# Kernel tuning notes

Measured on AMD Instinct MI355X. Metric: run time of the kernel, lower is better.

The kernel has to match this reference:

```python
import jax, jax.numpy as jnp
import numpy as np


def _conv(x, w, b, stride, pad):
    # x: [N,C,H,W], w: [O,I,kh,kw]
    y = jax.lax.conv_general_dilated(
        x, w, (stride, stride), [(pad, pad), (pad, pad)],
        dimension_numbers=('NCHW', 'OIHW', 'NCHW'))
    return y + b[None, :, None, None]


def _block(x, w1, b1, w2, b2, stride):
    # BasicBlock with BN folded: conv3x3 -> relu -> conv3x3
    h = jax.nn.relu(_conv(x, w1, b1, stride, 1))
    return _conv(h, w2, b2, 1, 1)


def setup_inputs() -> dict:
    key = jax.random.key(0)
    keys = iter(jax.random.split(key, 64))

    def rn(shape):
        fan_in = int(np.prod(shape[1:])) if len(shape) > 1 else shape[0]
        return jax.random.normal(next(keys), shape, jnp.float32) * (1.0 / np.sqrt(fan_in))

    d = {}
    d['inputs'] = jax.random.normal(next(keys), (128, 3, 64, 64), jnp.float32)
    d['probs'] = jax.random.uniform(next(keys), (128, 15), jnp.float32)
    d['seed_w'] = rn((64, 3, 3, 3))
    d['seed_b'] = jnp.zeros((64,), jnp.float32)
    specs = [(64, 64), (64, 128), (128, 256)]  # (cin, cout) per group
    for g, (ci, co) in enumerate(specs):
        d[f'g{g}_ds_w'] = rn((co, ci, 1, 1))
        d[f'g{g}_ds_b'] = jnp.zeros((co,), jnp.float32)
        d[f'g{g}_b0_w1'] = rn((co, ci, 3, 3))
        d[f'g{g}_b0_b1'] = jnp.zeros((co,), jnp.float32)
        d[f'g{g}_b0_w2'] = rn((co, co, 3, 3))
        d[f'g{g}_b0_b2'] = jnp.zeros((co,), jnp.float32)
        d[f'g{g}_r_w1'] = rn((4, co, co, 3, 3))
        d[f'g{g}_r_b1'] = jnp.zeros((4, co), jnp.float32)
        d[f'g{g}_r_w2'] = rn((4, co, co, 3, 3))
        d[f'g{g}_r_b2'] = jnp.zeros((4, co), jnp.float32)
    d['fc_w'] = rn((1000, 256))
    d['fc_b'] = jnp.zeros((1000,), jnp.float32)
    return d


def reference(inputs, probs, seed_w, seed_b,
              g0_ds_w, g0_ds_b, g0_b0_w1, g0_b0_b1, g0_b0_w2, g0_b0_b2,
              g0_r_w1, g0_r_b1, g0_r_w2, g0_r_b2,
              g1_ds_w, g1_ds_b, g1_b0_w1, g1_b0_b1, g1_b0_w2, g1_b0_b2,
              g1_r_w1, g1_r_b1, g1_r_w2, g1_r_b2,
              g2_ds_w, g2_ds_b, g2_b0_w1, g2_b0_b1, g2_b0_w2, g2_b0_b2,
              g2_r_w1, g2_r_b1, g2_r_w2, g2_r_b2,
              fc_w, fc_b):
    # policy[k, n] in {0,1}: hard-threshold of agent probs at 0.5 (forward_real)
    policy = jnp.where(probs < 0.5, 0.0, 1.0).astype(inputs.dtype).T  # [15, B]
    x = jax.nn.relu(_conv(inputs, seed_w, seed_b, 1, 1))
    groups = [
        (g0_ds_w, g0_ds_b, g0_b0_w1, g0_b0_b1, g0_b0_w2, g0_b0_b2, g0_r_w1, g0_r_b1, g0_r_w2, g0_r_b2, 1),
        (g1_ds_w, g1_ds_b, g1_b0_w1, g1_b0_b1, g1_b0_w2, g1_b0_b2, g1_r_w1, g1_r_b1, g1_r_w2, g1_r_b2, 2),
        (g2_ds_w, g2_ds_b, g2_b0_w1, g2_b0_b1, g2_b0_w2, g2_b0_b2, g2_r_w1, g2_r_b1, g2_r_w2, g2_r_b2, 2),
    ]
    idx = 0
    for (ds_w, ds_b, b0_w1, b0_b1, b0_w2, b0_b2, r_w1, r_b1, r_w2, r_b2, s) in groups:
        # first block of the group: strided, with 1x1 downsample residual
        residual = _conv(x, ds_w, ds_b, s, 0)
        fx = _block(x, b0_w1, b0_b1, b0_w2, b0_b2, s)
        m = policy[idx][:, None, None, None]
        idx += 1
        x = m * jax.nn.relu(residual + fx) + (1.0 - m) * residual
        # remaining 4 identity-residual blocks
        for j in range(4):
            residual = x
            fx = _block(x, r_w1[j], r_b1[j], r_w2[j], r_b2[j], 1)
            m = policy[idx][:, None, None, None]
            idx += 1
            x = m * jax.nn.relu(residual + fx) + (1.0 - m) * residual
    pooled = x.mean(axis=(2, 3))  # global average pool [B, 256]
    return pooled @ fc_w.T + fc_b
```

## Files before the change

### kernel.cpp

```cpp
#include <hip/hip_runtime.h>

using bf = unsigned short;
typedef __attribute__((ext_vector_type(8))) short short8v;
typedef __attribute__((ext_vector_type(4))) float f32x4;
typedef __attribute__((ext_vector_type(4))) unsigned int u32x4;
typedef __attribute__((ext_vector_type(2))) unsigned int u32x2;

__device__ __forceinline__ float bf2f(bf u) { return __uint_as_float(((unsigned)u) << 16); }
__device__ __forceinline__ bf f2bf(float f) {
    unsigned x = __float_as_uint(f);
    x += 0x7fffu + ((x >> 16) & 1u);
    return (bf)(x >> 16);
}

__device__ __forceinline__ void gload16(const bf* g, bf* l) {
    __builtin_amdgcn_global_load_lds(
        (const __attribute__((address_space(1))) void*)g,
        (__attribute__((address_space(3))) void*)l, 16, 0, 0);
}

template <int CI, int CC, int RS, int STRIDE, bool SEED, bool RELU, int CMB,
          int TH, int TW, int W>
__global__ __launch_bounds__(256, 3) void conv_mfma(
    const bf* __restrict__ X, const float* __restrict__ Xf,
    const bf* __restrict__ Wp, const float* __restrict__ bias,
    bf* __restrict__ Y, const bf* __restrict__ res,
    const float* __restrict__ probs, const bf* __restrict__ zpage,
    int kidx, int Co) {
    constexpr int PAD = (RS == 3) ? 1 : 0;
    constexpr int IN_ROWS = (TH - 1) * STRIDE + RS;
    constexpr int IN_COLS = (TW - 1) * STRIDE + RS;
    constexpr int NG = CC / 8;
    constexpr int HIN = W * STRIDE;
    constexpr int RSRS = RS * RS;
    constexpr int NCH = CI / CC;
    constexpr bool DIRECT = (RS == 1);
    constexpr int TG = IN_ROWS * IN_COLS * NG;
    constexpr int NITER = (TG + 255) / 256;
    constexpr int NPX = TH * TW;
    constexpr int NF = NPX / 32;
    constexpr int TPR = W / TW;
    constexpr int KSH = (STRIDE == 2) ? 1 : 0;
    constexpr int HALF = IN_ROWS * IN_COLS * CC;
    constexpr bool DBUF = (!DIRECT) && (!SEED) && (NCH > 1) && (2 * HALF * 2 <= 65536);

    __shared__ bf sX[DIRECT ? 8 : (DBUF ? 2 * HALF : HALF)];

    const int tid = threadIdx.x;
    const int n = blockIdx.z;
    const int coBase = blockIdx.y << 6;
    const int bx = blockIdx.x;
    const int tr0 = (bx / TPR) * TH;
    const int tc0 = (bx % TPR) * TW;

    bool active = true;
    if (kidx >= 0) active = (probs[n * 15 + kidx] >= 0.5f);
    if (!active) return;

    const int lane = tid & 63;
    const int wid = tid >> 6;
    const int l15 = lane & 15;
    const int lq = lane >> 4;
    const int wm = wid >> 1;
    const int wn = wid & 1;

    f32x4 acc[2][NF] = {};
    int prow[NF], pcol[NF];
#pragma unroll
    for (int nf = 0; nf < NF; ++nf) {
        int p = wn * (NPX / 2) + nf * 16 + l15;
        prow[nf] = p / TW;
        pcol[nf] = p % TW;
    }

    const bf* Xn = X + (size_t)n * HIN * HIN * CI;

    if constexpr (DIRECT) {
#pragma unroll
        for (int ch = 0; ch < NCH; ++ch) {
#pragma unroll
            for (int kk = 0; kk < CC / 32; ++kk) {
                short8v a[2], b[NF];
#pragma unroll
                for (int mf = 0; mf < 2; ++mf) {
                    int co = coBase + wm * 32 + mf * 16 + l15;
                    a[mf] = *reinterpret_cast<const short8v*>(
                        Wp + ((size_t)ch * Co + co) * CC + kk * 32 + lq * 8);
                }
#pragma unroll
                for (int nf = 0; nf < NF; ++nf) {
                    b[nf] = *reinterpret_cast<const short8v*>(
                        Xn + ((size_t)((tr0 + prow[nf]) * STRIDE) * HIN +
                              (tc0 + pcol[nf]) * STRIDE) * CI + ch * CC + kk * 32 + lq * 8);
                }
#pragma unroll
                for (int mf = 0; mf < 2; ++mf)
#pragma unroll
                    for (int nf = 0; nf < NF; ++nf)
                        acc[mf][nf] = __builtin_amdgcn_mfma_f32_16x16x32_bf16(
                            a[mf], b[nf], acc[mf][nf], 0, 0, 0);
            }
        }
    } else {
        auto stage = [&](int ch, bf* buf) {
            if constexpr (SEED) {
                const float* Xfn = Xf + (size_t)n * 3 * HIN * HIN;
                if (tid < TG) {
                    int ir = tid / IN_COLS;
                    int ic = tid % IN_COLS;
                    int in_r = tr0 - PAD + ir;
                    int in_c = tc0 - PAD + ic;
                    u32x4 u = {0, 0, 0, 0};
                    if ((unsigned)in_r < (unsigned)HIN && (unsigned)in_c < (unsigned)HIN) {
                        const float* p = Xfn + (size_t)in_r * HIN + in_c;
                        u[0] = (unsigned)f2bf(p[0]) | ((unsigned)f2bf(p[HIN * HIN]) << 16);
                        u[1] = (unsigned)f2bf(p[2 * HIN * HIN]);
                    }
                    *reinterpret_cast<u32x4*>(&buf[(size_t)tid * 8]) = u;
                }
            } else {
#pragma unroll
                for (int i = 0; i < NITER; ++i) {
                    int g = tid + i * 256;
                    if (TG % 256 == 0 || g < TG) {
                        int ir = g / (IN_COLS * NG);
                        int rem = g - ir * (IN_COLS * NG);
                        int ic = rem / NG;
                        int gc = rem - ic * NG;
                        int in_r = tr0 * STRIDE - PAD + ir;
                        int in_c = tc0 * STRIDE - PAD + ic;
                        int gsrc = gc ^ ((ic >> KSH) & (NG - 1));
                        const bf* src = zpage;
                        if ((unsigned)in_r < (unsigned)HIN && (unsigned)in_c < (unsigned)HIN)
                            src = Xn + ((size_t)in_r * HIN + in_c) * CI + ch * CC + gsrc * 8;
                        gload16(src, &buf[(size_t)g * 8]);
                    }
                }
            }
        };

        auto compute = [&](int ch, const bf* buf) {
            if constexpr (CC >= 32) {
#pragma unroll
                for (int j = 0; j < RSRS; ++j) {
                    const int dh = j / RS;
                    const int dw = j % RS;
#pragma unroll
                    for (int kk = 0; kk < CC / 32; ++kk) {
                        short8v a[2], b[NF];
#pragma unroll
                        for (int mf = 0; mf < 2; ++mf) {
                            int co = coBase + wm * 32 + mf * 16 + l15;
                            a[mf] = *reinterpret_cast<const short8v*>(
                                Wp + (((size_t)(ch * RSRS + j) * Co + co) * CC + kk * 32 + lq * 8));
                        }
#pragma unroll
                        for (int nf = 0; nf < NF; ++nf) {
                            int ir = prow[nf] * STRIDE + dh;
                            int ic = pcol[nf] * STRIDE + dw;
                            int gk = (kk * 4 + lq) ^ ((ic >> KSH) & (NG - 1));
                            b[nf] = *reinterpret_cast<const short8v*>(
                                &buf[((ir * IN_COLS + ic) * NG + gk) * 8]);
                        }
#pragma unroll
                        for (int mf = 0; mf < 2; ++mf)
#pragma unroll
                            for (int nf = 0; nf < NF; ++nf)
                                acc[mf][nf] = __builtin_amdgcn_mfma_f32_16x16x32_bf16(
                                    a[mf], b[nf], acc[mf][nf], 0, 0, 0);
                    }
                }
            } else {
#pragma unroll
                for (int kt = 0; kt < 3; ++kt) {
                    int j = kt * 4 + lq;
                    int jj = (j < 9) ? j : 0;
                    int dh = jj / 3, dw = jj % 3;
                    short8v a[2], b[NF];
#pragma unroll
                    for (int mf = 0; mf < 2; ++mf) {
                        int co = coBase + wm * 32 + mf * 16 + l15;
                        a[mf] = *reinterpret_cast<const short8v*>(Wp + ((size_t)j * Co + co) * 8);
                    }
#pragma unroll
                    for (int nf = 0; nf < NF; ++nf) {
                        int ir = prow[nf] + dh;
                        int ic = pcol[nf] + dw;
                        b[nf] = *reinterpret_cast<const short8v*>(&buf[(ir * IN_COLS + ic) * 8]);
                    }
#pragma unroll
                    for (int mf = 0; mf < 2; ++mf)
#pragma unroll
                        for (int nf = 0; nf < NF; ++nf)
                            acc[mf][nf] = __builtin_amdgcn_mfma_f32_16x16x32_bf16(
                                a[mf], b[nf], acc[mf][nf], 0, 0, 0);
                }
            }
        };

        if constexpr (DBUF) {
            stage(0, sX);
            __syncthreads();
#pragma unroll
            for (int ch = 0; ch < NCH; ++ch) {
                bf* cur = sX + (size_t)(ch & 1) * HALF;
                bf* nxt = sX + (size_t)((ch + 1) & 1) * HALF;
                if (ch + 1 < NCH) stage(ch + 1, nxt);
                compute(ch, cur);
                if (ch + 1 < NCH) __syncthreads();
            }
        } else {
            for (int ch = 0; ch < NCH; ++ch) {
                if (ch) __syncthreads();
                stage(ch, sX);
                __syncthreads();
                compute(ch, sX);
            }
        }
    }

#pragma unroll
    for (int mf = 0; mf < 2; ++mf) {
        int co0 = coBase + wm * 32 + mf * 16 + lq * 4;
        float4 b4 = *reinterpret_cast<const float4*>(bias + co0);
        float bb[4] = {b4.x, b4.y, b4.z, b4.w};
#pragma unroll
        for (int nf = 0; nf < NF; ++nf) {
            size_t off = ((size_t)n * W * W + (size_t)(tr0 + prow[nf]) * W + tc0 + pcol[nf]) * Co + co0;
            float v[4];
#pragma unroll
            for (int i = 0; i < 4; ++i) v[i] = acc[mf][nf][i] + bb[i];
            if constexpr (CMB >= 1) {
                u32x2 r2 = *reinterpret_cast<const u32x2*>(res + off);
                bf rr[4] = {(bf)(r2[0] & 0xffff), (bf)(r2[0] >> 16),
                            (bf)(r2[1] & 0xffff), (bf)(r2[1] >> 16)};
#pragma unroll
                for (int i = 0; i < 4; ++i) v[i] = fmaxf(v[i] + bf2f(rr[i]), 0.f);
            }
            if constexpr (RELU) {
#pragma unroll
                for (int i = 0; i < 4; ++i) v[i] = fmaxf(v[i], 0.f);
            }
            unsigned lo = (unsigned)f2bf(v[0]) | ((unsigned)f2bf(v[1]) << 16);
            unsigned hi = (unsigned)f2bf(v[2]) | ((unsigned)f2bf(v[3]) << 16);
            u32x2 o2 = {lo, hi};
            *reinterpret_cast<u32x2*>(Y + off) = o2;
        }
    }
}

#define NSEG 34
struct Seg {
    const float* src;
    bf* dst;
    int Co, Ci, RSRS, CC, JPAD, blk0;
};
struct SegArgs {
    Seg s[NSEG];
    bf* zpage;
};
__global__ void repack_all(SegArgs A) {
    int b = blockIdx.x;
    if (b == 0 && threadIdx.x < 16) {
        u32x4 z = {0, 0, 0, 0};
        *reinterpret_cast<u32x4*>(A.zpage + (size_t)threadIdx.x * 8) = z;
    }
    int lo = 0;
#pragma unroll 1
    for (int i = 1; i < NSEG; ++i)
        if (A.s[i].blk0 <= b) lo = i;
    Seg sg = A.s[lo];
    int NCH_ = (sg.Ci + sg.CC - 1) / sg.CC;
    size_t total8 = ((size_t)NCH_ * sg.JPAD * sg.Co * sg.CC) >> 3;
    size_t i8 = (size_t)(b - sg.blk0) * 256 + threadIdx.x;
    if (i8 >= total8) return;
    size_t e = i8 * 8;
    int cw = (int)(e % sg.CC);
    int co = (int)((e / sg.CC) % sg.Co);
    int j = (int)((e / ((size_t)sg.CC * sg.Co)) % sg.JPAD);
    int ch = (int)(e / ((size_t)sg.CC * sg.Co * sg.JPAD));
    bf tmp[8];
#pragma unroll
    for (int k = 0; k < 8; ++k) {
        int ci = ch * sg.CC + cw + k;
        float v = 0.f;
        if (ci < sg.Ci && j < sg.RSRS) v = sg.src[((size_t)co * sg.Ci + ci) * sg.RSRS + j];
        tmp[k] = f2bf(v);
    }
    u32x4 o;
#pragma unroll
    for (int k = 0; k < 4; ++k) o[k] = (unsigned)tmp[2 * k] | ((unsigned)tmp[2 * k + 1] << 16);
    *reinterpret_cast<u32x4*>(sg.dst + e) = o;
}

__global__ void poolfc_k(const bf* __restrict__ X, const float* __restrict__ fw,
                         const float* __restrict__ fb, float* __restrict__ out) {
    __shared__ float red[8][256];
    __shared__ float sp[256];
    int n = blockIdx.x;
    int g = threadIdx.x & 31;
    int slice = threadIdx.x >> 5;
    float acc[8] = {};
    for (int p = slice * 32; p < slice * 32 + 32; ++p) {
        u32x4 v = *reinterpret_cast<const u32x4*>(X + ((size_t)n * 256 + p) * 256 + g * 8);
#pragma unroll
        for (int i = 0; i < 4; ++i) {
            acc[2 * i] += bf2f((bf)(v[i] & 0xffff));
            acc[2 * i + 1] += bf2f((bf)(v[i] >> 16));
        }
    }
#pragma unroll
    for (int i = 0; i < 8; ++i) red[slice][g * 8 + i] = acc[i];
    __syncthreads();
    if (slice == 0) {
#pragma unroll
        for (int i = 0; i < 8; ++i) {
            float s = 0.f;
#pragma unroll
            for (int ss = 0; ss < 8; ++ss) s += red[ss][g * 8 + i];
            sp[g * 8 + i] = s * (1.f / 256.f);
        }
    }
    __syncthreads();
    for (int o = threadIdx.x; o < 1000; o += 256) {
        float a = fb[o];
        for (int k = 0; k < 256; ++k) a += sp[k] * fw[(size_t)o * 256 + k];
        out[(size_t)n * 1000 + o] = a;
    }
}

template <int CIN, int COUT, int S, int TH, int TW, int W, int CC1>
static void run_group(hipStream_t st, bf* X, bf* H, bf* OUT, const bf* zp,
                      bf* wp_ds, const float* ds_b, bf* wp_w1, const float* b1,
                      bf* wp_w2, const float* b2, bf* const* wp_rw1, const float* rb1,
                      bf* const* wp_rw2, const float* rb2, const float* probs_c,
                      int kbase, int NB) {
    dim3 grid((W / TH) * (W / TW), COUT / 64, NB);
    conv_mfma<CIN, 64, 1, S, false, false, 0, TH, TW, W><<<grid, 256, 0, st>>>(
        X, nullptr, wp_ds, ds_b, OUT, nullptr, nullptr, zp, -1, COUT);
    conv_mfma<CIN, CC1, 3, S, false, true, 0, TH, TW, W><<<grid, 256, 0, st>>>(
        X, nullptr, wp_w1, b1, H, nullptr, probs_c, zp, kbase, COUT);
    conv_mfma<COUT, 64, 3, 1, false, false, 2, TH, TW, W><<<grid, 256, 0, st>>>(
        H, nullptr, wp_w2, b2, OUT, OUT, probs_c, zp, kbase, COUT);
    for (int j = 0; j < 4; ++j) {
        conv_mfma<COUT, 64, 3, 1, false, true, 0, TH, TW, W><<<grid, 256, 0, st>>>(
            OUT, nullptr, wp_rw1[j], rb1 + j * COUT, H, nullptr, probs_c, zp,
            kbase + 1 + j, COUT);
        conv_mfma<COUT, 64, 3, 1, false, false, 2, TH, TW, W><<<grid, 256, 0, st>>>(
            H, nullptr, wp_rw2[j], rb2 + j * COUT, OUT, OUT, probs_c, zp,
            kbase + 1 + j, COUT);
    }
}

extern "C" void kernel_launch(void* const* d_in, const int* in_sizes, int n_in,
                              void* d_out, int out_size, void* d_ws, size_t ws_size,
                              hipStream_t stream) {
    (void)in_sizes; (void)n_in; (void)out_size;
    const float* input = (const float*)d_in[0];
    const float* probs = (const float*)d_in[1];
    const float* seed_w = (const float*)d_in[2];
    const float* seed_b = (const float*)d_in[3];
    const float* fc_w = (const float*)d_in[34];
    const float* fc_b = (const float*)d_in[35];

    char* pw = (char*)d_ws;
    auto alloc = [&](size_t bytes) -> void* {
        void* r = (void*)pw;
        pw += ((bytes + 255) & ~(size_t)255);
        return r;
    };

    bf* zpage = (bf*)alloc(256);

    SegArgs sa;
    sa.zpage = zpage;
    int nseg = 0;
    int blkAcc = 0;
    auto pack = [&](const float* w, int Co_, int Ci_, int RSRS_, int CC_, int JPAD_) -> bf* {
        int NCH_ = (Ci_ + CC_ - 1) / CC_;
        size_t total = (size_t)NCH_ * JPAD_ * Co_ * CC_;
        bf* wp = (bf*)alloc(total * 2);
        sa.s[nseg] = {w, wp, Co_, Ci_, RSRS_, CC_, JPAD_, blkAcc};
        blkAcc += (int)(((total >> 3) + 255) / 256);
        ++nseg;
        return wp;
    };

    bf* wpSeed = pack(seed_w, 64, 3, 9, 8, 12);
    const int cis[3] = {64, 64, 128};
    const int cos[3] = {64, 128, 256};
    const int cc1s[3] = {64, 32, 32};
    bf* wp_ds[3];
    bf* wp_w1[3];
    bf* wp_w2[3];
    bf* wp_rw1[3][4];
    bf* wp_rw2[3][4];
    const float *ds_b[3], *b1[3], *b2[3], *rb1[3], *rb2[3];
    for (int g = 0; g < 3; ++g) {
        int base = 4 + g * 10;
        const float* dsw = (const float*)d_in[base + 0];
        ds_b[g] = (const float*)d_in[base + 1];
        const float* w1 = (const float*)d_in[base + 2];
        b1[g] = (const float*)d_in[base + 3];
        const float* w2 = (const float*)d_in[base + 4];
        b2[g] = (const float*)d_in[base + 5];
        const float* rw1 = (const float*)d_in[base + 6];
        rb1[g] = (const float*)d_in[base + 7];
        const float* rw2 = (const float*)d_in[base + 8];
        rb2[g] = (const float*)d_in[base + 9];
        int Ci = cis[g], Co = cos[g];
        wp_ds[g] = pack(dsw, Co, Ci, 1, 64, 1);
        wp_w1[g] = pack(w1, Co, Ci, 9, cc1s[g], 9);
        wp_w2[g] = pack(w2, Co, Co, 9, 64, 9);
        for (int j = 0; j < 4; ++j) {
            wp_rw1[g][j] = pack(rw1 + (size_t)j * Co * Co * 9, Co, Co, 9, 64, 9);
            wp_rw2[g][j] = pack(rw2 + (size_t)j * Co * Co * 9, Co, Co, 9, 64, 9);
        }
    }
    for (int i = nseg; i < NSEG; ++i) sa.s[i] = {nullptr, nullptr, 1, 1, 1, 1, 1, 0x7fffffff};
    repack_all<<<dim3(blkAcc), 256, 0, stream>>>(sa);

    size_t used = (size_t)(pw - (char*)d_ws);
    size_t avail = (ws_size > used) ? (ws_size - used) : 0;
    const size_t PER_IMG = 64ull * 64 * 64 * 2;
    int NB = 128;
    while (NB > 8 && (size_t)3 * NB * PER_IMG + 4096 > avail) NB >>= 1;

    bf* A = (bf*)alloc((size_t)NB * PER_IMG);
    bf* Bb = (bf*)alloc((size_t)NB * PER_IMG);
    bf* C = (bf*)alloc((size_t)NB * PER_IMG);

    for (int n0 = 0; n0 < 128; n0 += NB) {
        const float* pc = probs + (size_t)n0 * 15;
        conv_mfma<8, 8, 3, 1, true, true, 0, 8, 16, 64><<<dim3(32, 1, NB), 256, 0, stream>>>(
            nullptr, input + (size_t)n0 * 3 * 4096, wpSeed, seed_b, A, nullptr,
            nullptr, zpage, -1, 64);

        run_group<64, 64, 1, 8, 16, 64, 64>(stream, A, Bb, C, zpage,
                                            wp_ds[0], ds_b[0], wp_w1[0], b1[0],
                                            wp_w2[0], b2[0], wp_rw1[0], rb1[0],
                                            wp_rw2[0], rb2[0], pc, 0, NB);
        run_group<64, 128, 2, 8, 16, 32, 32>(stream, C, Bb, A, zpage,
                                             wp_ds[1], ds_b[1], wp_w1[1], b1[1],
                                             wp_w2[1], b2[1], wp_rw1[1], rb1[1],
                                             wp_rw2[1], rb2[1], pc, 5, NB);
        run_group<128, 256, 2, 8, 8, 16, 32>(stream, A, Bb, C, zpage,
                                             wp_ds[2], ds_b[2], wp_w1[2], b1[2],
                                             wp_w2[2], b2[2], wp_rw1[2], rb1[2],
                                             wp_rw2[2], rb2[2], pc, 10, NB);

        poolfc_k<<<dim3(NB), 256, 0, stream>>>(C, fc_w, fc_b,
                                               (float*)d_out + (size_t)n0 * 1000);
    }
}
```

Before: 2.217 ms.

## Stage full input-channel tiles in LDS once and retune conv tile shapes

Each conv now stages all input channels of its spatial tile into shared memory in one pass, with one barrier, instead of looping over 64- or 32-channel chunks. This removes the double-buffered chunk pipeline and the extra barriers. Weights are repacked with chunk size equal to the full channel count. Tile shapes are retuned per group, with separate tiles for the strided first convs and the stride-1 convs. In exchange, load/compute overlap is lost and the larger LDS footprints (up to about 51KB) may reduce occupancy.

```diff
diff --git a/kernel.cpp b/kernel.cpp
--- a/kernel.cpp
+++ b/kernel.cpp
@@ -41,10 +41,8 @@
     constexpr int NF = NPX / 32;
     constexpr int TPR = W / TW;
     constexpr int KSH = (STRIDE == 2) ? 1 : 0;
-    constexpr int HALF = IN_ROWS * IN_COLS * CC;
-    constexpr bool DBUF = (!DIRECT) && (!SEED) && (NCH > 1) && (2 * HALF * 2 <= 65536);
-
-    __shared__ bf sX[DIRECT ? 8 : (DBUF ? 2 * HALF : HALF)];
+
+    __shared__ bf sX[DIRECT ? 8 : IN_ROWS * IN_COLS * CC];
 
     const int tid = threadIdx.x;
     const int n = blockIdx.z;
@@ -102,91 +100,88 @@
             }
         }
     } else {
-        auto stage = [&](int ch, bf* buf) {
-            if constexpr (SEED) {
-                const float* Xfn = Xf + (size_t)n * 3 * HIN * HIN;
-                if (tid < TG) {
-                    int ir = tid / IN_COLS;
-                    int ic = tid % IN_COLS;
-                    int in_r = tr0 - PAD + ir;
-                    int in_c = tc0 - PAD + ic;
-                    u32x4 u = {0, 0, 0, 0};
-                    if ((unsigned)in_r < (unsigned)HIN && (unsigned)in_c < (unsigned)HIN) {
-                        const float* p = Xfn + (size_t)in_r * HIN + in_c;
-                        u[0] = (unsigned)f2bf(p[0]) | ((unsigned)f2bf(p[HIN * HIN]) << 16);
-                        u[1] = (unsigned)f2bf(p[2 * HIN * HIN]);
-                    }
-                    *reinterpret_cast<u32x4*>(&buf[(size_t)tid * 8]) = u;
-                }
-            } else {
-#pragma unroll
-                for (int i = 0; i < NITER; ++i) {
-                    int g = tid + i * 256;
-                    if (TG % 256 == 0 || g < TG) {
-                        int ir = g / (IN_COLS * NG);
-                        int rem = g - ir * (IN_COLS * NG);
-                        int ic = rem / NG;
-                        int gc = rem - ic * NG;
-                        int in_r = tr0 * STRIDE - PAD + ir;
-                        int in_c = tc0 * STRIDE - PAD + ic;
-                        int gsrc = gc ^ ((ic >> KSH) & (NG - 1));
-                        const bf* src = zpage;
-                        if ((unsigned)in_r < (unsigned)HIN && (unsigned)in_c < (unsigned)HIN)
-                            src = Xn + ((size_t)in_r * HIN + in_c) * CI + ch * CC + gsrc * 8;
-                        gload16(src, &buf[(size_t)g * 8]);
-                    }
-                }
-            }
-        };
-
-        auto compute = [&](int ch, const bf* buf) {
-            if constexpr (CC >= 32) {
-#pragma unroll
-                for (int j = 0; j < RSRS; ++j) {
-                    const int dh = j / RS;
-                    const int dw = j % RS;
-#pragma unroll
-                    for (int kk = 0; kk < CC / 32; ++kk) {
-                        short8v a[2], b[NF];
-#pragma unroll
-                        for (int mf = 0; mf < 2; ++mf) {
-                            int co = coBase + wm * 32 + mf * 16 + l15;
-                            a[mf] = *reinterpret_cast<const short8v*>(
-                                Wp + (((size_t)(ch * RSRS + j) * Co + co) * CC + kk * 32 + lq * 8));
-                        }
-#pragma unroll
-                        for (int nf = 0; nf < NF; ++nf) {
-                            int ir = prow[nf] * STRIDE + dh;
-                            int ic = pcol[nf] * STRIDE + dw;
-                            int gk = (kk * 4 + lq) ^ ((ic >> KSH) & (NG - 1));
-                            b[nf] = *reinterpret_cast<const short8v*>(
-                                &buf[((ir * IN_COLS + ic) * NG + gk) * 8]);
-                        }
-#pragma unroll
-                        for (int mf = 0; mf < 2; ++mf)
-#pragma unroll
-                            for (int nf = 0; nf < NF; ++nf)
-                                acc[mf][nf] = __builtin_amdgcn_mfma_f32_16x16x32_bf16(
-                                    a[mf], b[nf], acc[mf][nf], 0, 0, 0);
-                    }
-                }
-            } else {
-#pragma unroll
-                for (int kt = 0; kt < 3; ++kt) {
-                    int j = kt * 4 + lq;
-                    int jj = (j < 9) ? j : 0;
-                    int dh = jj / 3, dw = jj % 3;
+        if constexpr (SEED) {
+            const float* Xfn = Xf + (size_t)n * 3 * HIN * HIN;
+            if (tid < TG) {
+                int ir = tid / IN_COLS;
+                int ic = tid % IN_COLS;
+                int in_r = tr0 - PAD + ir;
+                int in_c = tc0 - PAD + ic;
+                u32x4 u = {0, 0, 0, 0};
+                if ((unsigned)in_r < (unsigned)HIN && (unsigned)in_c < (unsigned)HIN) {
+                    const float* p = Xfn + (size_t)in_r * HIN + in_c;
+                    u[0] = (unsigned)f2bf(p[0]) | ((unsigned)f2bf(p[HIN * HIN]) << 16);
+                    u[1] = (unsigned)f2bf(p[2 * HIN * HIN]);
+                }
+                *reinterpret_cast<u32x4*>(&sX[(size_t)tid * 8]) = u;
+            }
+        } else {
+#pragma unroll
+            for (int i = 0; i < NITER; ++i) {
+                int g = tid + i * 256;
+                if (TG % 256 == 0 || g < TG) {
+                    int ir = g / (IN_COLS * NG);
+                    int rem = g - ir * (IN_COLS * NG);
+                    int ic = rem / NG;
+                    int gc = rem - ic * NG;
+                    int in_r = tr0 * STRIDE - PAD + ir;
+                    int in_c = tc0 * STRIDE - PAD + ic;
+                    int gsrc = gc ^ ((ic >> KSH) & (NG - 1));
+                    const bf* src = zpage;
+                    if ((unsigned)in_r < (unsigned)HIN && (unsigned)in_c < (unsigned)HIN)
+                        src = Xn + ((size_t)in_r * HIN + in_c) * CI + gsrc * 8;
+                    gload16(src, &sX[(size_t)g * 8]);
+                }
+            }
+        }
+        __syncthreads();
+
+        if constexpr (SEED) {
+#pragma unroll
+            for (int kt = 0; kt < 3; ++kt) {
+                int j = kt * 4 + lq;
+                int jj = (j < 9) ? j : 0;
+                int dh = jj / 3, dw = jj % 3;
+                short8v a[2], b[NF];
+#pragma unroll
+                for (int mf = 0; mf < 2; ++mf) {
+                    int co = coBase + wm * 32 + mf * 16 + l15;
+                    a[mf] = *reinterpret_cast<const short8v*>(Wp + ((size_t)j * Co + co) * 8);
+                }
+#pragma unroll
+                for (int nf = 0; nf < NF; ++nf) {
+                    int ir = prow[nf] + dh;
+                    int ic = pcol[nf] + dw;
+                    b[nf] = *reinterpret_cast<const short8v*>(&sX[(ir * IN_COLS + ic) * 8]);
+                }
+#pragma unroll
+                for (int mf = 0; mf < 2; ++mf)
+#pragma unroll
+                    for (int nf = 0; nf < NF; ++nf)
+                        acc[mf][nf] = __builtin_amdgcn_mfma_f32_16x16x32_bf16(
+                            a[mf], b[nf], acc[mf][nf], 0, 0, 0);
+            }
+        } else {
+#pragma unroll
+            for (int j = 0; j < RSRS; ++j) {
+                const int dh = j / RS;
+                const int dw = j % RS;
+#pragma unroll
+                for (int kk = 0; kk < CC / 32; ++kk) {
                     short8v a[2], b[NF];
 #pragma unroll
                     for (int mf = 0; mf < 2; ++mf) {
                         int co = coBase + wm * 32 + mf * 16 + l15;
-                        a[mf] = *reinterpret_cast<const short8v*>(Wp + ((size_t)j * Co + co) * 8);
+                        a[mf] = *reinterpret_cast<const short8v*>(
+                            Wp + (((size_t)j * Co + co) * CC + kk * 32 + lq * 8));
                     }
 #pragma unroll
                     for (int nf = 0; nf < NF; ++nf) {
-                        int ir = prow[nf] + dh;
-                        int ic = pcol[nf] + dw;
-                        b[nf] = *reinterpret_cast<const short8v*>(&buf[(ir * IN_COLS + ic) * 8]);
+                        int ir = prow[nf] * STRIDE + dh;
+                        int ic = pcol[nf] * STRIDE + dw;
+                        int gk = (kk * 4 + lq) ^ ((ic >> KSH) & (NG - 1));
+                        b[nf] = *reinterpret_cast<const short8v*>(
+                            &sX[((ir * IN_COLS + ic) * NG + gk) * 8]);
                     }
 #pragma unroll
                     for (int mf = 0; mf < 2; ++mf)
@@ -195,26 +190,6 @@
                             acc[mf][nf] = __builtin_amdgcn_mfma_f32_16x16x32_bf16(
                                 a[mf], b[nf], acc[mf][nf], 0, 0, 0);
                 }
-            }
-        };
-
-        if constexpr (DBUF) {
-            stage(0, sX);
-            __syncthreads();
-#pragma unroll
-            for (int ch = 0; ch < NCH; ++ch) {
-                bf* cur = sX + (size_t)(ch & 1) * HALF;
-                bf* nxt = sX + (size_t)((ch + 1) & 1) * HALF;
-                if (ch + 1 < NCH) stage(ch + 1, nxt);
-                compute(ch, cur);
-                if (ch + 1 < NCH) __syncthreads();
-            }
-        } else {
-            for (int ch = 0; ch < NCH; ++ch) {
-                if (ch) __syncthreads();
-                stage(ch, sX);
-                __syncthreads();
-                compute(ch, sX);
             }
         }
     }
@@ -329,24 +304,25 @@
     }
 }
 
-template <int CIN, int COUT, int S, int TH, int TW, int W, int CC1>
+template <int CIN, int COUT, int S, int TH1, int TW1, int TH2, int TW2, int W>
 static void run_group(hipStream_t st, bf* X, bf* H, bf* OUT, const bf* zp,
                       bf* wp_ds, const float* ds_b, bf* wp_w1, const float* b1,
                       bf* wp_w2, const float* b2, bf* const* wp_rw1, const float* rb1,
                       bf* const* wp_rw2, const float* rb2, const float* probs_c,
                       int kbase, int NB) {
-    dim3 grid((W / TH) * (W / TW), COUT / 64, NB);
-    conv_mfma<CIN, 64, 1, S, false, false, 0, TH, TW, W><<<grid, 256, 0, st>>>(
+    dim3 grid1((W / TH1) * (W / TW1), COUT / 64, NB);
+    dim3 grid2((W / TH2) * (W / TW2), COUT / 64, NB);
+    conv_mfma<CIN, CIN, 1, S, false, false, 0, TH2, TW2, W><<<grid2, 256, 0, st>>>(
         X, nullptr, wp_ds, ds_b, OUT, nullptr, nullptr, zp, -1, COUT);
-    conv_mfma<CIN, CC1, 3, S, false, true, 0, TH, TW, W><<<grid, 256, 0, st>>>(
+    conv_mfma<CIN, CIN, 3, S, false, true, 0, TH2, TW2, W><<<grid2, 256, 0, st>>>(
         X, nullptr, wp_w1, b1, H, nullptr, probs_c, zp, kbase, COUT);
-    conv_mfma<COUT, 64, 3, 1, false, false, 2, TH, TW, W><<<grid, 256, 0, st>>>(
+    conv_mfma<COUT, COUT, 3, 1, false, false, 2, TH1, TW1, W><<<grid1, 256, 0, st>>>(
         H, nullptr, wp_w2, b2, OUT, OUT, probs_c, zp, kbase, COUT);
     for (int j = 0; j < 4; ++j) {
-        conv_mfma<COUT, 64, 3, 1, false, true, 0, TH, TW, W><<<grid, 256, 0, st>>>(
+        conv_mfma<COUT, COUT, 3, 1, false, true, 0, TH1, TW1, W><<<grid1, 256, 0, st>>>(
             OUT, nullptr, wp_rw1[j], rb1 + j * COUT, H, nullptr, probs_c, zp,
             kbase + 1 + j, COUT);
-        conv_mfma<COUT, 64, 3, 1, false, false, 2, TH, TW, W><<<grid, 256, 0, st>>>(
+        conv_mfma<COUT, COUT, 3, 1, false, false, 2, TH1, TW1, W><<<grid1, 256, 0, st>>>(
             H, nullptr, wp_rw2[j], rb2 + j * COUT, OUT, OUT, probs_c, zp,
             kbase + 1 + j, COUT);
     }
@@ -389,7 +365,6 @@
     bf* wpSeed = pack(seed_w, 64, 3, 9, 8, 12);
     const int cis[3] = {64, 64, 128};
     const int cos[3] = {64, 128, 256};
-    const int cc1s[3] = {64, 32, 32};
     bf* wp_ds[3];
     bf* wp_w1[3];
     bf* wp_w2[3];
@@ -409,12 +384,12 @@
         const float* rw2 = (const float*)d_in[base + 8];
         rb2[g] = (const float*)d_in[base + 9];
         int Ci = cis[g], Co = cos[g];
-        wp_ds[g] = pack(dsw, Co, Ci, 1, 64, 1);
-        wp_w1[g] = pack(w1, Co, Ci, 9, cc1s[g], 9);
-        wp_w2[g] = pack(w2, Co, Co, 9, 64, 9);
+        wp_ds[g] = pack(dsw, Co, Ci, 1, Ci, 1);
+        wp_w1[g] = pack(w1, Co, Ci, 9, Ci, 9);
+        wp_w2[g] = pack(w2, Co, Co, 9, Co, 9);
         for (int j = 0; j < 4; ++j) {
-            wp_rw1[g][j] = pack(rw1 + (size_t)j * Co * Co * 9, Co, Co, 9, 64, 9);
-            wp_rw2[g][j] = pack(rw2 + (size_t)j * Co * Co * 9, Co, Co, 9, 64, 9);
+            wp_rw1[g][j] = pack(rw1 + (size_t)j * Co * Co * 9, Co, Co, 9, Co, 9);
+            wp_rw2[g][j] = pack(rw2 + (size_t)j * Co * Co * 9, Co, Co, 9, Co, 9);
         }
     }
     for (int i = nseg; i < NSEG; ++i) sa.s[i] = {nullptr, nullptr, 1, 1, 1, 1, 1, 0x7fffffff};
@@ -436,18 +411,18 @@
             nullptr, input + (size_t)n0 * 3 * 4096, wpSeed, seed_b, A, nullptr,
             nullptr, zpage, -1, 64);
 
-        run_group<64, 64, 1, 8, 16, 64, 64>(stream, A, Bb, C, zpage,
-                                            wp_ds[0], ds_b[0], wp_w1[0], b1[0],
-                                            wp_w2[0], b2[0], wp_rw1[0], rb1[0],
-                                            wp_rw2[0], rb2[0], pc, 0, NB);
-        run_group<64, 128, 2, 8, 16, 32, 32>(stream, C, Bb, A, zpage,
-                                             wp_ds[1], ds_b[1], wp_w1[1], b1[1],
-                                             wp_w2[1], b2[1], wp_rw1[1], rb1[1],
-                                             wp_rw2[1], rb2[1], pc, 5, NB);
-        run_group<128, 256, 2, 8, 8, 16, 32>(stream, A, Bb, C, zpage,
-                                             wp_ds[2], ds_b[2], wp_w1[2], b1[2],
-                                             wp_w2[2], b2[2], wp_rw1[2], rb1[2],
-                                             wp_rw2[2], rb2[2], pc, 10, NB);
+        run_group<64, 64, 1, 8, 16, 8, 16, 64>(stream, A, Bb, C, zpage,
+                                               wp_ds[0], ds_b[0], wp_w1[0], b1[0],
+                                               wp_w2[0], b2[0], wp_rw1[0], rb1[0],
+                                               wp_rw2[0], rb2[0], pc, 0, NB);
+        run_group<64, 128, 2, 8, 8, 8, 8, 32>(stream, C, Bb, A, zpage,
+                                              wp_ds[1], ds_b[1], wp_w1[1], b1[1],
+                                              wp_w2[1], b2[1], wp_rw1[1], rb1[1],
+                                              wp_rw2[1], rb2[1], pc, 5, NB);
+        run_group<128, 256, 2, 8, 8, 8, 4, 16>(stream, A, Bb, C, zpage,
+                                               wp_ds[2], ds_b[2], wp_w1[2], b1[2],
+                                               wp_w2[2], b2[2], wp_rw1[2], rb1[2],
+                                               wp_rw2[2], rb2[2], pc, 10, NB);
 
         poolfc_k<<<dim3(NB), 256, 0, stream>>>(C, fc_w, fc_b,
                                                (float*)d_out + (size_t)n0 * 1000);
```

New measurement: 2.401 ms. 1.08x slower.
